# Performance work log

Measured on AMD Instinct MI355X. Metric: run time of the kernel, lower is better.

## Reference

```python
import jax, jax.numpy as jnp
import numpy as np

N_NODES = 50000
N_EDGES = 1000000
N_HID = 64
N_GRAPHS = 500
IN_DIM = 4


def setup_inputs() -> dict:
    key = jax.random.key(0)
    ks = jax.random.split(key, 10)
    x = jax.random.normal(ks[0], (N_NODES, IN_DIM), dtype=jnp.float32)
    edge_index = jax.random.randint(ks[1], (2, N_EDGES), 0, N_NODES, dtype=jnp.int64)
    batch = jnp.sort(jax.random.randint(ks[2], (N_NODES,), 0, N_GRAPHS, dtype=jnp.int64))
    # learned parameters (glorot-ish init)
    W1 = jax.random.normal(ks[3], (IN_DIM, N_HID), dtype=jnp.float32) / np.sqrt(IN_DIM)
    b1 = jnp.zeros((N_HID,), dtype=jnp.float32)
    W2 = jax.random.normal(ks[4], (N_HID, N_HID), dtype=jnp.float32) / np.sqrt(N_HID)
    b2 = jnp.zeros((N_HID,), dtype=jnp.float32)
    W3 = jax.random.normal(ks[5], (N_HID, 1), dtype=jnp.float32) / np.sqrt(N_HID)
    b3 = jnp.zeros((1,), dtype=jnp.float32)
    return {"x": x, "edge_index": edge_index, "batch": batch,
            "W1": W1, "b1": b1, "W2": W2, "b2": b2, "W3": W3, "b3": b3}


def gcn_conv(x, W, b, src, dst, num_nodes):
    """PyG GCNConv: x@W, add self-loops, sym deg^-1/2 norm, scatter-add aggregate, +bias."""
    h = x @ W  # [N, D]
    loop = jnp.arange(num_nodes, dtype=src.dtype)
    s = jnp.concatenate([src, loop])  # source nodes (messages gathered from)
    d = jnp.concatenate([dst, loop])  # target nodes (messages scattered to)
    deg = jax.ops.segment_sum(jnp.ones_like(d, dtype=h.dtype), d, num_segments=num_nodes)
    dis = jnp.where(deg > 0, jax.lax.rsqrt(jnp.maximum(deg, 1e-12)), 0.0)
    norm = dis[s] * dis[d]  # [E+N]
    msg = h[s] * norm[:, None]  # gather + scale: the memory-bound hot loop
    out = jax.ops.segment_sum(msg, d, num_segments=num_nodes)
    return out + b


def reference(x, edge_index, batch, W1, b1, W2, b2, W3, b3):
    src, dst = edge_index[0], edge_index[1]
    n = x.shape[0]
    h = gcn_conv(x, W1, b1, src, dst, n)
    h = jax.nn.elu(h)
    # F.dropout with training=False (eval mode) is identity
    h = gcn_conv(h, W2, b2, src, dst, n)
    h = jax.nn.elu(h)
    # scatter-mean pooling over graphs
    sums = jax.ops.segment_sum(h, batch, num_segments=N_GRAPHS)
    cnts = jax.ops.segment_sum(jnp.ones((n,), dtype=h.dtype), batch, num_segments=N_GRAPHS)
    pooled = sums / jnp.maximum(cnts, 1.0)[:, None]
    return pooled @ W3 + b3  # [N_GRAPHS, 1]
```

## Files before the change

kernel.cpp:

```cpp
#include <hip/hip_runtime.h>
#include <hip/hip_fp16.h>
#include <math.h>

#define N_NODES 50000
#define N_EDGES 1000000
#define N_HID 64
#define N_GRAPHS 500
#define IN_DIM 4
#define NPAD 50048

#define BK_SHIFT 7
#define BK_NODES 128
#define NBUCK 391
#define BCAP 3072
#define EPT 16
#define EPW (EPT * 256)
#define NWG_BIN ((N_EDGES + EPW - 1) / EPW)

__global__ void k_init(int* bcur, int* gstart, int* gend, float* sums) {
    int i = blockIdx.x * blockDim.x + threadIdx.x;
    if (i < 512) { bcur[i] = 0; gstart[i] = 0; gend[i] = 0; }
    if (i < N_GRAPHS * N_HID) sums[i] = 0.f;
}

__global__ void k_bin(const int* __restrict__ ei, int* bcur, int* __restrict__ P) {
    __shared__ int hist[NBUCK];
    __shared__ int base[NBUCK];
    int t = threadIdx.x;
    int wg0 = blockIdx.x * EPW;
    for (int b = t; b < NBUCK; b += 256) hist[b] = 0;
    __syncthreads();

    const int4* s4 = (const int4*)ei;
    const int4* d4 = (const int4*)(ei + N_EDGES);
    int rs[EPT], rd[EPT], rl[EPT];
#pragma unroll
    for (int i = 0; i < 4; ++i) {
        int e = wg0 + (i * 256 + t) * 4;
        if (e < N_EDGES) {
            int4 vs = s4[e >> 2];
            int4 vd = d4[e >> 2];
            rs[i * 4 + 0] = vs.x; rd[i * 4 + 0] = vd.x;
            rs[i * 4 + 1] = vs.y; rd[i * 4 + 1] = vd.y;
            rs[i * 4 + 2] = vs.z; rd[i * 4 + 2] = vd.z;
            rs[i * 4 + 3] = vs.w; rd[i * 4 + 3] = vd.w;
            rl[i * 4 + 0] = atomicAdd(&hist[vd.x >> BK_SHIFT], 1);
            rl[i * 4 + 1] = atomicAdd(&hist[vd.y >> BK_SHIFT], 1);
            rl[i * 4 + 2] = atomicAdd(&hist[vd.z >> BK_SHIFT], 1);
            rl[i * 4 + 3] = atomicAdd(&hist[vd.w >> BK_SHIFT], 1);
        } else {
            rd[i * 4 + 0] = rd[i * 4 + 1] = rd[i * 4 + 2] = rd[i * 4 + 3] = -1;
        }
    }
    __syncthreads();
    for (int b = t; b < NBUCK; b += 256) {
        int h = hist[b];
        base[b] = h ? atomicAdd(&bcur[b], h) : 0;
    }
    __syncthreads();
#pragma unroll
    for (int i = 0; i < EPT; ++i) {
        if (rd[i] >= 0) {
            int bk = rd[i] >> BK_SHIFT;
            int loc = base[bk] + rl[i];
            if (loc > BCAP - 1) loc = BCAP - 1;
            P[(size_t)bk * BCAP + loc] = (rs[i] << BK_SHIFT) | (rd[i] & (BK_NODES - 1));
        }
    }
}

__global__ void k_build(const int* __restrict__ bcur, const int* __restrict__ P,
                        const float* __restrict__ x,
                        int* __restrict__ srcidx, int* __restrict__ offs,
                        int* __restrict__ endp, float* __restrict__ dis,
                        float* __restrict__ xs) {
    __shared__ int sp[BCAP];
    __shared__ int scnt[BK_NODES];
    __shared__ int sscan[BK_NODES];
    __shared__ int scur[BK_NODES];
    int b = blockIdx.x;
    int t = threadIdx.x;
    int n = bcur[b];
    if (n > BCAP) n = BCAP;
    if (t < BK_NODES) scnt[t] = 0;
    __syncthreads();
    for (int i = t; i < n; i += 256) {
        int v = P[(size_t)b * BCAP + i];
        sp[i] = v;
        atomicAdd(&scnt[v & (BK_NODES - 1)], 1);
    }
    __syncthreads();
    if (t < BK_NODES) sscan[t] = scnt[t];
    __syncthreads();
    for (int d = 1; d < BK_NODES; d <<= 1) {
        int v = 0;
        if (t < BK_NODES && t >= d) v = sscan[t - d];
        __syncthreads();
        if (t < BK_NODES) sscan[t] += v;
        __syncthreads();
    }
    if (t < BK_NODES) {
        int excl = sscan[t] - scnt[t];
        scur[t] = excl;
        int node = b * BK_NODES + t;
        if (node < N_NODES) {
            int o = b * BCAP + excl;
            offs[node] = o;
            endp[node] = o + scnt[t];
            float dd = 1.0f / sqrtf((float)(scnt[t] + 1));
            dis[node] = dd;
            float4 xv = ((const float4*)x)[node];
            xv.x *= dd; xv.y *= dd; xv.z *= dd; xv.w *= dd;
            ((float4*)xs)[node] = xv;
        }
    }
    __syncthreads();
    for (int i = t; i < n; i += 256) {
        int v = sp[i];
        int ln = v & (BK_NODES - 1);
        int pos = b * BCAP + atomicAdd(&scur[ln], 1);
        srcidx[pos] = v >> BK_SHIFT;
    }
}

__global__ void k_layer1(const float* __restrict__ xs, const int* __restrict__ offs,
                         const int* __restrict__ endp, const int* __restrict__ srcidx,
                         const float* __restrict__ dis, const int* __restrict__ batch,
                         const float* __restrict__ W1, const float* __restrict__ b1,
                         int* __restrict__ gstart, int* __restrict__ gend,
                         __half* __restrict__ h1s) {
    __shared__ float4 sagg[256];
    __shared__ float sdis[256];
    __shared__ float sW1[IN_DIM * N_HID];
    __shared__ float sb1[N_HID];
    int t = threadIdx.x;
    int nb = blockIdx.x * 256;
    int i = nb + t;
    sW1[t] = W1[t];
    if (t < N_HID) sb1[t] = b1[t];
    if (i < N_NODES) {
        int g = batch[i];
        if (i == 0 || batch[i - 1] != g) gstart[g] = i;
        if (i == N_NODES - 1 || batch[i + 1] != g) gend[g] = i + 1;
        const float4* xs4 = (const float4*)xs;
        float4 a0 = xs4[i];
        float4 a1 = make_float4(0.f, 0.f, 0.f, 0.f);
        float4 a2 = a1, a3 = a1;
        int q = offs[i], e = endp[i];
        for (; q + 4 <= e; q += 4) {
            int i0 = srcidx[q], i1 = srcidx[q + 1], i2 = srcidx[q + 2], i3 = srcidx[q + 3];
            float4 v0 = xs4[i0], v1 = xs4[i1], v2 = xs4[i2], v3 = xs4[i3];
            a0.x += v0.x; a0.y += v0.y; a0.z += v0.z; a0.w += v0.w;
            a1.x += v1.x; a1.y += v1.y; a1.z += v1.z; a1.w += v1.w;
            a2.x += v2.x; a2.y += v2.y; a2.z += v2.z; a2.w += v2.w;
            a3.x += v3.x; a3.y += v3.y; a3.z += v3.z; a3.w += v3.w;
        }
        for (; q < e; ++q) {
            float4 v = xs4[srcidx[q]];
            a0.x += v.x; a0.y += v.y; a0.z += v.z; a0.w += v.w;
        }
        float dd = dis[i];
        float4 r;
        r.x = (a0.x + a1.x + a2.x + a3.x) * dd;
        r.y = (a0.y + a1.y + a2.y + a3.y) * dd;
        r.z = (a0.z + a1.z + a2.z + a3.z) * dd;
        r.w = (a0.w + a1.w + a2.w + a3.w) * dd;
        sagg[t] = r;
        sdis[t] = dd;
    } else {
        sagg[t] = make_float4(0.f, 0.f, 0.f, 0.f);
        sdis[t] = 0.f;
    }
    __syncthreads();
    int w = t >> 6, j = t & 63;
    float w0 = sW1[0 * N_HID + j], w1 = sW1[1 * N_HID + j];
    float w2 = sW1[2 * N_HID + j], w3 = sW1[3 * N_HID + j];
    float bj = sb1[j];
    for (int n = 0; n < 64; ++n) {
        int local = w * 64 + n;
        int node = nb + local;
        if (node >= N_NODES) break;
        float4 a = sagg[local];
        float acc = a.x * w0 + a.y * w1 + a.z * w2 + a.w * w3 + bj;
        acc = acc > 0.f ? acc : expm1f(acc);
        h1s[(size_t)node * N_HID + j] = __float2half_rn(acc * sdis[local]);
    }
}

__device__ inline void acc_half8(float* acc, float4 raw) {
    const __half2* hp = (const __half2*)&raw;
#pragma unroll
    for (int c = 0; c < 4; ++c) {
        float2 f = __half22float2(hp[c]);
        acc[2 * c + 0] += f.x;
        acc[2 * c + 1] += f.y;
    }
}

__global__ void k_agg16(const __half* __restrict__ h1s, const int* __restrict__ offs,
                        const int* __restrict__ endp, const int* __restrict__ srcidx,
                        const float* __restrict__ dis, float* __restrict__ tmp2) {
    int wid = (blockIdx.x * blockDim.x + threadIdx.x) >> 6;
    int lane = threadIdx.x & 63;
    int g = lane >> 3, l = lane & 7;
    if (wid >= N_NODES) return;
    const float4* hsv = (const float4*)h1s;
    float accA[8] = {0.f, 0.f, 0.f, 0.f, 0.f, 0.f, 0.f, 0.f};
    float accB[8] = {0.f, 0.f, 0.f, 0.f, 0.f, 0.f, 0.f, 0.f};
    if (g == 0) acc_half8(accA, hsv[(size_t)wid * 8 + l]);
    int start = offs[wid], end = endp[wid];
    for (int base = start; base < end; base += 64) {
        int nc = end - base; if (nc > 64) nc = 64;
        int myidx = (base + lane < end) ? srcidx[base + lane] : 0;
        int q = 0;
        for (; q + 16 <= nc; q += 16) {
            int s0 = __shfl(myidx, q + g);
            int s1 = __shfl(myidx, q + 8 + g);
            float4 r0 = hsv[(size_t)s0 * 8 + l];
            float4 r1 = hsv[(size_t)s1 * 8 + l];
            acc_half8(accA, r0);
            acc_half8(accB, r1);
        }
        if (q + 8 <= nc) {
            int s = __shfl(myidx, q + g);
            acc_half8(accA, hsv[(size_t)s * 8 + l]);
            q += 8;
        }
        {
            int s = __shfl(myidx, q + g);
            if (q + g < nc) acc_half8(accB, hsv[(size_t)s * 8 + l]);
        }
    }
#pragma unroll
    for (int c = 0; c < 8; ++c) accA[c] += accB[c];
#pragma unroll
    for (int c = 0; c < 8; ++c) {
        accA[c] += __shfl_xor(accA[c], 8);
        accA[c] += __shfl_xor(accA[c], 16);
        accA[c] += __shfl_xor(accA[c], 32);
    }
    if (g == 0) {
        float dw = dis[wid];
        float4 v0 = make_float4(accA[0] * dw, accA[1] * dw, accA[2] * dw, accA[3] * dw);
        float4 v1 = make_float4(accA[4] * dw, accA[5] * dw, accA[6] * dw, accA[7] * dw);
        ((float4*)tmp2)[(size_t)wid * 16 + 2 * l] = v0;
        ((float4*)tmp2)[(size_t)wid * 16 + 2 * l + 1] = v1;
    }
}

#define GP_NODES 64
__global__ void k_gemmpool(const float* __restrict__ tmp2, const int* __restrict__ batch,
                           const float* __restrict__ W2, const float* __restrict__ b2,
                           float* __restrict__ sums) {
    __shared__ float sAT[N_HID][68];
    __shared__ int sbat[GP_NODES];
    int t = threadIdx.x;
    int nb = blockIdx.x * GP_NODES;
    if (t < GP_NODES) sbat[t] = (nb + t < N_NODES) ? batch[nb + t] : -1;
    {
        int sn = t >> 2, k0 = (t & 3) * 16;
        int node = nb + sn;
        bool ok = node < N_NODES;
        const float4* a4 = (const float4*)&tmp2[(size_t)(ok ? node : 0) * N_HID];
#pragma unroll
        for (int i = 0; i < 4; ++i) {
            float4 v = ok ? a4[k0 / 4 + i] : make_float4(0.f, 0.f, 0.f, 0.f);
            sAT[k0 + 4 * i + 0][sn] = v.x;
            sAT[k0 + 4 * i + 1][sn] = v.y;
            sAT[k0 + 4 * i + 2][sn] = v.z;
            sAT[k0 + 4 * i + 3][sn] = v.w;
        }
    }
    __syncthreads();
    int tj = t & 15, tn = t >> 4;
    const float4* W2v = (const float4*)W2;
    float4 acc0 = make_float4(0.f, 0.f, 0.f, 0.f);
    float4 acc1 = acc0, acc2 = acc0, acc3 = acc0;
#pragma unroll 8
    for (int k = 0; k < N_HID; ++k) {
        float4 a = *(const float4*)&sAT[k][4 * tn];
        float4 w = W2v[k * 16 + tj];
        acc0.x += a.x * w.x; acc0.y += a.x * w.y; acc0.z += a.x * w.z; acc0.w += a.x * w.w;
        acc1.x += a.y * w.x; acc1.y += a.y * w.y; acc1.z += a.y * w.z; acc1.w += a.y * w.w;
        acc2.x += a.z * w.x; acc2.y += a.z * w.y; acc2.z += a.z * w.z; acc2.w += a.z * w.w;
        acc3.x += a.w * w.x; acc3.y += a.w * w.y; acc3.z += a.w * w.z; acc3.w += a.w * w.w;
    }
    float4 bb = ((const float4*)b2)[tj];
    __syncthreads();
#define GP_WB(ACC, I)                                                         \
    {                                                                         \
        float4 r;                                                             \
        r.x = ACC.x + bb.x; r.y = ACC.y + bb.y;                               \
        r.z = ACC.z + bb.z; r.w = ACC.w + bb.w;                               \
        r.x = r.x > 0.f ? r.x : expm1f(r.x);                                  \
        r.y = r.y > 0.f ? r.y : expm1f(r.y);                                  \
        r.z = r.z > 0.f ? r.z : expm1f(r.z);                                  \
        r.w = r.w > 0.f ? r.w : expm1f(r.w);                                  \
        sAT[4 * tj + 0][4 * tn + (I)] = r.x;                                  \
        sAT[4 * tj + 1][4 * tn + (I)] = r.y;                                  \
        sAT[4 * tj + 2][4 * tn + (I)] = r.z;                                  \
        sAT[4 * tj + 3][4 * tn + (I)] = r.w;                                  \
    }
    GP_WB(acc0, 0) GP_WB(acc1, 1) GP_WB(acc2, 2) GP_WB(acc3, 3)
#undef GP_WB
    __syncthreads();
    int j = t & 63, w = t >> 6;
    int s = 0;
    while (s < GP_NODES) {
        int gg = sbat[s];
        int e = s + 1;
        while (e < GP_NODES && sbat[e] == gg) ++e;
        if (gg >= 0 && s + w < e) {
            float p = 0.f;
            for (int n = s + w; n < e; n += 4) p += sAT[j][n];
            atomicAdd(&sums[gg * N_HID + j], p);
        }
        s = e;
    }
}

__global__ void k_final(const float* __restrict__ sums, const int* __restrict__ gstart,
                        const int* __restrict__ gend, const float* __restrict__ W3,
                        const float* __restrict__ b3, float* __restrict__ out) {
    int gid = blockIdx.x * 4 + (threadIdx.x >> 6);
    int j = threadIdx.x & 63;
    if (gid >= N_GRAPHS) return;
    int cnt = gend[gid] - gstart[gid];
    float v = sums[gid * N_HID + j] / (float)(cnt > 0 ? cnt : 1);
    float p = v * W3[j];
#pragma unroll
    for (int off = 32; off; off >>= 1) p += __shfl_down(p, off);
    if (j == 0) out[gid] = p + b3[0];
}

extern "C" void kernel_launch(void* const* d_in, const int* in_sizes, int n_in,
                              void* d_out, int out_size, void* d_ws, size_t ws_size,
                              hipStream_t stream) {
    const float* x   = (const float*)d_in[0];
    const int*   ei  = (const int*)d_in[1];
    const int*   bat = (const int*)d_in[2];
    const float* W1  = (const float*)d_in[3];
    const float* b1  = (const float*)d_in[4];
    const float* W2  = (const float*)d_in[5];
    const float* b2  = (const float*)d_in[6];
    const float* W3  = (const float*)d_in[7];
    const float* b3  = (const float*)d_in[8];
    float* out = (float*)d_out;

    char* w = (char*)d_ws;
    int*   bcur   = (int*)w;   w += 512 * 4;
    int*   offs   = (int*)w;   w += NPAD * 4;
    int*   endp   = (int*)w;   w += NPAD * 4;
    float* dis    = (float*)w; w += NPAD * 4;
    int*   gstart = (int*)w;   w += 512 * 4;
    int*   gend   = (int*)w;   w += 512 * 4;
    float* sums   = (float*)w; w += (size_t)N_GRAPHS * N_HID * 4;
    float* xs     = (float*)w; w += (size_t)NPAD * IN_DIM * 4;
    int*   srcidx = (int*)w;   w += (size_t)NBUCK * BCAP * 4;
    int*   P      = (int*)w;   w += (size_t)NBUCK * BCAP * 4;
    __half* h1s   = (__half*)w; w += (size_t)N_NODES * N_HID * 2;
    float* tmp2   = (float*)w; w += (size_t)N_NODES * N_HID * 4;

    const int B = 256;
    const int gN = (N_NODES + B - 1) / B;
    const int gW = (N_NODES * 64 + B - 1) / B;

    k_init<<<(N_GRAPHS * N_HID + B - 1) / B, B, 0, stream>>>(bcur, gstart, gend, sums);
    k_bin<<<NWG_BIN, B, 0, stream>>>(ei, bcur, P);
    k_build<<<NBUCK, B, 0, stream>>>(bcur, P, x, srcidx, offs, endp, dis, xs);

    k_layer1<<<gN, B, 0, stream>>>(xs, offs, endp, srcidx, dis, bat, W1, b1,
                                   gstart, gend, h1s);

    k_agg16<<<gW, B, 0, stream>>>(h1s, offs, endp, srcidx, dis, tmp2);
    k_gemmpool<<<(N_NODES + GP_NODES - 1) / GP_NODES, B, 0, stream>>>(
        tmp2, bat, W2, b2, sums);

    k_final<<<(N_GRAPHS + 3) / 4, B, 0, stream>>>(sums, gstart, gend, W3, b3, out);
}
```

Measured before the change: 97.01 us.

## Split layer-2 aggregation into two passes by source-node half for cache locality

The build step now partitions each node's neighbor list into sources below and above a split point and records a mid offset. Layer-2 aggregation runs as two kernels, each gathering from only half of the fp16 feature table, so the gathered working set is more likely to stay in cache. The second pass reads back the partial sums and applies the normalization. Index loads and partial-sum stores use nontemporal hints. The cost is an extra launch, an extra read and write of the intermediate tensor, and duplicated per-node wave setup.

```diff
diff --git a/kernel.cpp b/kernel.cpp
--- a/kernel.cpp
+++ b/kernel.cpp
@@ -8,6 +8,7 @@
 #define N_GRAPHS 500
 #define IN_DIM 4
 #define NPAD 50048
+#define SRC_SPLIT 25000
 
 #define BK_SHIFT 7
 #define BK_NODES 128
@@ -16,6 +17,8 @@
 #define EPT 16
 #define EPW (EPT * 256)
 #define NWG_BIN ((N_EDGES + EPW - 1) / EPW)
+
+typedef float nt_f4 __attribute__((ext_vector_type(4)));
 
 __global__ void k_init(int* bcur, int* gstart, int* gend, float* sums) {
     int i = blockIdx.x * blockDim.x + threadIdx.x;
@@ -72,22 +75,26 @@
 __global__ void k_build(const int* __restrict__ bcur, const int* __restrict__ P,
                         const float* __restrict__ x,
                         int* __restrict__ srcidx, int* __restrict__ offs,
-                        int* __restrict__ endp, float* __restrict__ dis,
-                        float* __restrict__ xs) {
+                        int* __restrict__ mid, int* __restrict__ endp,
+                        float* __restrict__ dis, float* __restrict__ xs) {
     __shared__ int sp[BCAP];
     __shared__ int scnt[BK_NODES];
+    __shared__ int scntLo[BK_NODES];
     __shared__ int sscan[BK_NODES];
-    __shared__ int scur[BK_NODES];
+    __shared__ int scurLo[BK_NODES];
+    __shared__ int scurHi[BK_NODES];
     int b = blockIdx.x;
     int t = threadIdx.x;
     int n = bcur[b];
     if (n > BCAP) n = BCAP;
-    if (t < BK_NODES) scnt[t] = 0;
+    if (t < BK_NODES) { scnt[t] = 0; scntLo[t] = 0; }
     __syncthreads();
     for (int i = t; i < n; i += 256) {
         int v = P[(size_t)b * BCAP + i];
         sp[i] = v;
-        atomicAdd(&scnt[v & (BK_NODES - 1)], 1);
+        int ln = v & (BK_NODES - 1);
+        atomicAdd(&scnt[ln], 1);
+        if ((v >> BK_SHIFT) < SRC_SPLIT) atomicAdd(&scntLo[ln], 1);
     }
     __syncthreads();
     if (t < BK_NODES) sscan[t] = scnt[t];
@@ -101,11 +108,13 @@
     }
     if (t < BK_NODES) {
         int excl = sscan[t] - scnt[t];
-        scur[t] = excl;
+        scurLo[t] = excl;
+        scurHi[t] = excl + scntLo[t];
         int node = b * BK_NODES + t;
         if (node < N_NODES) {
             int o = b * BCAP + excl;
             offs[node] = o;
+            mid[node] = o + scntLo[t];
             endp[node] = o + scnt[t];
             float dd = 1.0f / sqrtf((float)(scnt[t] + 1));
             dis[node] = dd;
@@ -118,8 +127,10 @@
     for (int i = t; i < n; i += 256) {
         int v = sp[i];
         int ln = v & (BK_NODES - 1);
-        int pos = b * BCAP + atomicAdd(&scur[ln], 1);
-        srcidx[pos] = v >> BK_SHIFT;
+        int src = v >> BK_SHIFT;
+        int pos = b * BCAP + ((src < SRC_SPLIT) ? atomicAdd(&scurLo[ln], 1)
+                                                : atomicAdd(&scurHi[ln], 1));
+        srcidx[pos] = src;
     }
 }
 
@@ -197,9 +208,71 @@
     }
 }
 
-__global__ void k_agg16(const __half* __restrict__ h1s, const int* __restrict__ offs,
-                        const int* __restrict__ endp, const int* __restrict__ srcidx,
-                        const float* __restrict__ dis, float* __restrict__ tmp2) {
+__device__ inline void gather_range(const float4* __restrict__ hsv,
+                                    const int* __restrict__ srcidx,
+                                    int start, int end, int lane, int g, int l,
+                                    float* accA, float* accB) {
+    for (int base = start; base < end; base += 64) {
+        int nc = end - base; if (nc > 64) nc = 64;
+        int myidx = (base + lane < end)
+                        ? __builtin_nontemporal_load(&srcidx[base + lane]) : 0;
+        int q = 0;
+        for (; q + 16 <= nc; q += 16) {
+            int s0 = __shfl(myidx, q + g);
+            int s1 = __shfl(myidx, q + 8 + g);
+            float4 r0 = hsv[(size_t)s0 * 8 + l];
+            float4 r1 = hsv[(size_t)s1 * 8 + l];
+            acc_half8(accA, r0);
+            acc_half8(accB, r1);
+        }
+        if (q + 8 <= nc) {
+            int s = __shfl(myidx, q + g);
+            acc_half8(accA, hsv[(size_t)s * 8 + l]);
+            q += 8;
+        }
+        {
+            int s = __shfl(myidx, q + g);
+            if (q + g < nc) acc_half8(accB, hsv[(size_t)s * 8 + l]);
+        }
+    }
+}
+
+__device__ inline void fold_groups(float* accA, const float* accB) {
+#pragma unroll
+    for (int c = 0; c < 8; ++c) accA[c] += accB[c];
+#pragma unroll
+    for (int c = 0; c < 8; ++c) {
+        accA[c] += __shfl_xor(accA[c], 8);
+        accA[c] += __shfl_xor(accA[c], 16);
+        accA[c] += __shfl_xor(accA[c], 32);
+    }
+}
+
+__global__ void k_agg_lo(const __half* __restrict__ h1s, const int* __restrict__ offs,
+                         const int* __restrict__ mid, const int* __restrict__ srcidx,
+                         float* __restrict__ tmp2) {
+    int wid = (blockIdx.x * blockDim.x + threadIdx.x) >> 6;
+    int lane = threadIdx.x & 63;
+    int g = lane >> 3, l = lane & 7;
+    if (wid >= N_NODES) return;
+    const float4* hsv = (const float4*)h1s;
+    float accA[8] = {0.f, 0.f, 0.f, 0.f, 0.f, 0.f, 0.f, 0.f};
+    float accB[8] = {0.f, 0.f, 0.f, 0.f, 0.f, 0.f, 0.f, 0.f};
+    gather_range(hsv, srcidx, offs[wid], mid[wid], lane, g, l, accA, accB);
+    fold_groups(accA, accB);
+    if (g == 0) {
+        nt_f4* t4 = (nt_f4*)tmp2;
+        nt_f4 v0, v1;
+        v0.x = accA[0]; v0.y = accA[1]; v0.z = accA[2]; v0.w = accA[3];
+        v1.x = accA[4]; v1.y = accA[5]; v1.z = accA[6]; v1.w = accA[7];
+        __builtin_nontemporal_store(v0, &t4[(size_t)wid * 16 + 2 * l]);
+        __builtin_nontemporal_store(v1, &t4[(size_t)wid * 16 + 2 * l + 1]);
+    }
+}
+
+__global__ void k_agg_hi(const __half* __restrict__ h1s, const int* __restrict__ mid,
+                         const int* __restrict__ endp, const int* __restrict__ srcidx,
+                         const float* __restrict__ dis, float* __restrict__ tmp2) {
     int wid = (blockIdx.x * blockDim.x + threadIdx.x) >> 6;
     int lane = threadIdx.x & 63;
     int g = lane >> 3, l = lane & 7;
@@ -208,43 +281,20 @@
     float accA[8] = {0.f, 0.f, 0.f, 0.f, 0.f, 0.f, 0.f, 0.f};
     float accB[8] = {0.f, 0.f, 0.f, 0.f, 0.f, 0.f, 0.f, 0.f};
     if (g == 0) acc_half8(accA, hsv[(size_t)wid * 8 + l]);
-    int start = offs[wid], end = endp[wid];
-    for (int base = start; base < end; base += 64) {
-        int nc = end - base; if (nc > 64) nc = 64;
-        int myidx = (base + lane < end) ? srcidx[base + lane] : 0;
-        int q = 0;
-        for (; q + 16 <= nc; q += 16) {
-            int s0 = __shfl(myidx, q + g);
-            int s1 = __shfl(myidx, q + 8 + g);
-            float4 r0 = hsv[(size_t)s0 * 8 + l];
-            float4 r1 = hsv[(size_t)s1 * 8 + l];
-            acc_half8(accA, r0);
-            acc_half8(accB, r1);
-        }
-        if (q + 8 <= nc) {
-            int s = __shfl(myidx, q + g);
-            acc_half8(accA, hsv[(size_t)s * 8 + l]);
-            q += 8;
-        }
-        {
-            int s = __shfl(myidx, q + g);
-            if (q + g < nc) acc_half8(accB, hsv[(size_t)s * 8 + l]);
-        }
-    }
-#pragma unroll
-    for (int c = 0; c < 8; ++c) accA[c] += accB[c];
-#pragma unroll
-    for (int c = 0; c < 8; ++c) {
-        accA[c] += __shfl_xor(accA[c], 8);
-        accA[c] += __shfl_xor(accA[c], 16);
-        accA[c] += __shfl_xor(accA[c], 32);
-    }
+    gather_range(hsv, srcidx, mid[wid], endp[wid], lane, g, l, accA, accB);
+    fold_groups(accA, accB);
     if (g == 0) {
+        nt_f4* t4 = (nt_f4*)tmp2;
+        nt_f4 p0 = __builtin_nontemporal_load(&t4[(size_t)wid * 16 + 2 * l]);
+        nt_f4 p1 = __builtin_nontemporal_load(&t4[(size_t)wid * 16 + 2 * l + 1]);
         float dw = dis[wid];
-        float4 v0 = make_float4(accA[0] * dw, accA[1] * dw, accA[2] * dw, accA[3] * dw);
-        float4 v1 = make_float4(accA[4] * dw, accA[5] * dw, accA[6] * dw, accA[7] * dw);
-        ((float4*)tmp2)[(size_t)wid * 16 + 2 * l] = v0;
-        ((float4*)tmp2)[(size_t)wid * 16 + 2 * l + 1] = v1;
+        nt_f4 v0, v1;
+        v0.x = (accA[0] + p0.x) * dw; v0.y = (accA[1] + p0.y) * dw;
+        v0.z = (accA[2] + p0.z) * dw; v0.w = (accA[3] + p0.w) * dw;
+        v1.x = (accA[4] + p1.x) * dw; v1.y = (accA[5] + p1.y) * dw;
+        v1.z = (accA[6] + p1.z) * dw; v1.w = (accA[7] + p1.w) * dw;
+        __builtin_nontemporal_store(v0, &t4[(size_t)wid * 16 + 2 * l]);
+        __builtin_nontemporal_store(v1, &t4[(size_t)wid * 16 + 2 * l + 1]);
     }
 }
 
@@ -350,6 +400,7 @@
     char* w = (char*)d_ws;
     int*   bcur   = (int*)w;   w += 512 * 4;
     int*   offs   = (int*)w;   w += NPAD * 4;
+    int*   mid    = (int*)w;   w += NPAD * 4;
     int*   endp   = (int*)w;   w += NPAD * 4;
     float* dis    = (float*)w; w += NPAD * 4;
     int*   gstart = (int*)w;   w += 512 * 4;
@@ -367,12 +418,13 @@
 
     k_init<<<(N_GRAPHS * N_HID + B - 1) / B, B, 0, stream>>>(bcur, gstart, gend, sums);
     k_bin<<<NWG_BIN, B, 0, stream>>>(ei, bcur, P);
-    k_build<<<NBUCK, B, 0, stream>>>(bcur, P, x, srcidx, offs, endp, dis, xs);
+    k_build<<<NBUCK, B, 0, stream>>>(bcur, P, x, srcidx, offs, mid, endp, dis, xs);
 
     k_layer1<<<gN, B, 0, stream>>>(xs, offs, endp, srcidx, dis, bat, W1, b1,
                                    gstart, gend, h1s);
 
-    k_agg16<<<gW, B, 0, stream>>>(h1s, offs, endp, srcidx, dis, tmp2);
+    k_agg_lo<<<gW, B, 0, stream>>>(h1s, offs, mid, srcidx, tmp2);
+    k_agg_hi<<<gW, B, 0, stream>>>(h1s, mid, endp, srcidx, dis, tmp2);
     k_gemmpool<<<(N_NODES + GP_NODES - 1) / GP_NODES, B, 0, stream>>>(
         tmp2, bat, W2, b2, sums);
 
```

Result: slower. 118.9 us (+22.5%).
